# Kernel optimization log

Hardware: AMD Instinct MI355X
Metric: run time of the kernel (lower is better)

## Reference

```python
import jax, jax.numpy as jnp
import numpy as np

N, E, G = 50000, 640000, 128
IN_DIM, LAT, H, HID, NC = 128, 32, 8, 128, 2


def setup_inputs() -> dict:
    key = jax.random.key(0)
    ks = jax.random.split(key, 16)
    x = jax.random.normal(ks[0], (N, IN_DIM), dtype=jnp.float32)
    edge_index = jax.random.randint(ks[1], (2, E), 0, N, dtype=jnp.int64)
    # contiguous graph blocks covering all G graph ids
    batch = (jnp.arange(N, dtype=jnp.int64) * G) // N
    y = jax.random.randint(ks[2], (G,), 0, NC, dtype=jnp.int64)

    def lin(k, fi, fo):
        return jax.random.normal(k, (fi, fo), dtype=jnp.float32) / np.sqrt(fi)

    return {
        'x': x, 'edge_index': edge_index, 'batch': batch, 'y': y,
        'W1': lin(ks[3], IN_DIM, LAT), 'b1': jnp.zeros((LAT,), jnp.float32),
        'Wg1': lin(ks[4], LAT, H * LAT),
        'asrc1': jax.random.normal(ks[5], (H, LAT), jnp.float32) / np.sqrt(LAT),
        'adst1': jax.random.normal(ks[6], (H, LAT), jnp.float32) / np.sqrt(LAT),
        'bg1': jnp.zeros((H * LAT,), jnp.float32),
        'Wg2': lin(ks[7], H * LAT, H * LAT),
        'asrc2': jax.random.normal(ks[8], (H, LAT), jnp.float32) / np.sqrt(LAT),
        'adst2': jax.random.normal(ks[9], (H, LAT), jnp.float32) / np.sqrt(LAT),
        'bg2': jnp.zeros((H * LAT,), jnp.float32),
        'Wl1': lin(ks[10], LAT + 2 * H * LAT, HID), 'bl1': jnp.zeros((HID,), jnp.float32),
        'Wl2': lin(ks[11], HID, NC), 'bl2': jnp.zeros((NC,), jnp.float32),
    }


def _add_self_loops(edge_index, n):
    loop = jnp.arange(n, dtype=edge_index.dtype)
    row = jnp.concatenate([edge_index[0], loop])
    col = jnp.concatenate([edge_index[1], loop])
    return row, col


def gcn_conv(x, row, col, W, b):
    h = x @ W  # [N, C]
    deg = jax.ops.segment_sum(jnp.ones_like(col, dtype=h.dtype), col, num_segments=N)
    dinv = jax.lax.rsqrt(jnp.maximum(deg, 1.0))  # self-loops guarantee deg >= 1
    norm = dinv[row] * dinv[col]  # [E']
    return jax.ops.segment_sum(norm[:, None] * h[row], col, num_segments=N) + b


def gat_conv(x, row, col, W, a_src, a_dst, b):
    h = (x @ W).reshape(N, H, LAT)  # [N, H, C]
    s = jnp.einsum('nhc,hc->nh', h, a_src)
    d = jnp.einsum('nhc,hc->nh', h, a_dst)
    logits = jax.nn.leaky_relu(s[row] + d[col], negative_slope=0.2)  # [E', H]
    m = jax.ops.segment_max(logits, col, num_segments=N)
    m = jnp.where(jnp.isfinite(m), m, 0.0)
    e = jnp.exp(logits - m[col])
    z = jax.ops.segment_sum(e, col, num_segments=N)
    alpha = e / (z[col] + 1e-16)  # segment softmax over incoming edges
    out = jax.ops.segment_sum(alpha[:, :, None] * h[row], col, num_segments=N)
    return out.reshape(N, H * LAT) + b


def reference(x, edge_index, batch, y, W1, b1, Wg1, asrc1, adst1, bg1,
              Wg2, asrc2, adst2, bg2, Wl1, bl1, Wl2, bl2):
    row, col = _add_self_loops(edge_index, N)
    h1 = jax.nn.elu(gcn_conv(x, row, col, W1, b1))
    h2 = jax.nn.elu(gat_conv(h1, row, col, Wg1, asrc1, adst1, bg1))
    h3 = jax.nn.elu(gat_conv(h2, row, col, Wg2, asrc2, adst2, bg2))
    cat = jnp.concatenate([h1, h2, h3], axis=1)  # [N, 544]
    # first node of each graph (batch is sorted, contiguous blocks)
    idx = jnp.searchsorted(batch, jnp.arange(G, dtype=batch.dtype))
    feature = cat[idx] @ Wl1 + bl1  # [G, HID]
    hidden = jax.nn.elu(feature)  # eval mode: dropout off
    raw = hidden @ Wl2 + bl2
    prob = jax.nn.softmax(raw, axis=1)
    logits = jax.nn.log_softmax(raw, axis=1)
    loss = -jnp.mean(jnp.take_along_axis(logits, y[:, None], axis=1))
    pred = jnp.argmax(logits, axis=1, keepdims=True)
    return logits, loss, pred, prob, feature
```

## Files before the change

### kernel.cpp

```cpp
#include <hip/hip_runtime.h>
#include <math.h>

#define NN 50000
#define EE 640000
#define EP (EE + NN)
#define GG 128
#define IND 128
#define LATC 32
#define HH 8
#define HLC 256
#define HIDN 128
#define SCAN_B 256
#define SCAN_G ((NN + SCAN_B - 1) / SCAN_B)

typedef unsigned short ushortT;
typedef unsigned int uintT;
typedef short bf16x8 __attribute__((ext_vector_type(8)));
typedef float f32x4 __attribute__((ext_vector_type(4)));

__device__ __forceinline__ float elu1(float v) { return v > 0.f ? v : (__expf(v) - 1.f); }

__device__ __forceinline__ ushortT f2bf(float f) {
  unsigned int u = __float_as_uint(f);
  return (ushortT)((u + 0x7fffu + ((u >> 16) & 1u)) >> 16);
}
__device__ __forceinline__ float bf2f(ushortT s) {
  return __uint_as_float(((unsigned int)s) << 16);
}

__global__ void init_kernel(int* cnt, int* cursor) {
  int t = blockIdx.x * blockDim.x + threadIdx.x;
  if (t < NN) { cnt[t] = 1; cursor[t] = 0; }
}

__global__ void count_kernel(const int* col, int* cnt) {
  int t = blockIdx.x * blockDim.x + threadIdx.x;
  if (t < EE) atomicAdd(&cnt[col[t]], 1);
}

__global__ void scan_part_kernel(const int* __restrict__ cnt,
                                 int* __restrict__ bsum) {
  int t = threadIdx.x;
  int i = blockIdx.x * SCAN_B + t;
  int v = (i < NN) ? cnt[i] : 0;
#pragma unroll
  for (int d = 1; d < 64; d <<= 1) v += __shfl_xor(v, d);
  __shared__ int ws[4];
  if ((t & 63) == 0) ws[t >> 6] = v;
  __syncthreads();
  if (t == 0) bsum[blockIdx.x] = ws[0] + ws[1] + ws[2] + ws[3];
}

__global__ void scan_top_kernel(const int* __restrict__ bsum,
                                int* __restrict__ ebsum,
                                int* __restrict__ offs_last) {
  int t = threadIdx.x;
  int v = (t < SCAN_G) ? bsum[t] : 0;
  int orig = v;
  int lane = t & 63, w = t >> 6;
#pragma unroll
  for (int d = 1; d < 64; d <<= 1) {
    int o = __shfl_up(v, d);
    if (lane >= d) v += o;
  }
  __shared__ int ws[4];
  if (lane == 63) ws[w] = v;
  __syncthreads();
  int add = 0;
  for (int j = 0; j < w; ++j) add += ws[j];
  v += add;
  if (t < SCAN_G) ebsum[t] = v - orig;
  if (t == SCAN_G - 1) *offs_last = v;
}

__global__ void scan_final_kernel(const int* __restrict__ cnt,
                                  const int* __restrict__ ebsum,
                                  int* __restrict__ offs,
                                  float* __restrict__ dinv) {
  int t = threadIdx.x;
  int i = blockIdx.x * SCAN_B + t;
  int v = (i < NN) ? cnt[i] : 0;
  int orig = v;
  int lane = t & 63, w = t >> 6;
#pragma unroll
  for (int d = 1; d < 64; d <<= 1) {
    int o = __shfl_up(v, d);
    if (lane >= d) v += o;
  }
  __shared__ int ws[4];
  if (lane == 63) ws[w] = v;
  __syncthreads();
  int add = ebsum[blockIdx.x];
  for (int j = 0; j < w; ++j) add += ws[j];
  if (i < NN) {
    offs[i] = v - orig + add;
    dinv[i] = 1.f / sqrtf((float)orig);
  }
}

__global__ void build_kernel(const int* row, const int* col, const int* offs,
                             int* cursor, int* srcs) {
  int t = blockIdx.x * blockDim.x + threadIdx.x;
  if (t >= EP) return;
  int r, c;
  if (t < EE) { r = row[t]; c = col[t]; } else { r = t - EE; c = r; }
  int pos = offs[c] + atomicAdd(&cursor[c], 1);
  srcs[pos] = r;
}

__global__ void finalize_kernel(const int* offs, int* srcs) {
  int gw = (blockIdx.x * blockDim.x + threadIdx.x) >> 6;
  if (gw >= NN) return;
  int lane = threadIdx.x & 63;
  int beg = offs[gw], end = offs[gw + 1];
  int deg = end - beg;
  if (deg <= 64) {
    int v = (lane < deg) ? srcs[beg + lane] : 0x7fffffff;
    for (int k = 2; k <= 64; k <<= 1)
      for (int j = k >> 1; j > 0; j >>= 1) {
        int o = __shfl_xor(v, j);
        bool keepmin = (((lane & k) == 0) == ((lane & j) == 0));
        v = keepmin ? (v < o ? v : o) : (v > o ? v : o);
      }
    if (lane < deg) srcs[beg + lane] = v;
  } else if (lane == 0) {
    for (int i = beg + 1; i < end; ++i) {
      int v = srcs[i]; int j = i - 1;
      while (j >= beg && srcs[j] > v) { srcs[j + 1] = srcs[j]; --j; }
      srcs[j + 1] = v;
    }
  }
}

__launch_bounds__(256)
__global__ void gemm_in_kernel(const float* __restrict__ A,
                               const float* __restrict__ W,
                               float* __restrict__ out) {
  __shared__ float As[IND][68];
  __shared__ float Bs[IND][LATC];
  int bm = blockIdx.x * 64;
  int tid = threadIdx.x;
  int tx = tid & 31, ty = tid >> 5;
  {
    const float4* Wv = (const float4*)W;
    float4* Bv = (float4*)Bs;
#pragma unroll
    for (int i = 0; i < 4; ++i) Bv[tid + i * 256] = Wv[tid + i * 256];
  }
  {
    int m = tid >> 2, k4 = (tid & 3) * 4;
    int gm = bm + m;
#pragma unroll
    for (int pass = 0; pass < 8; ++pass) {
      int k = pass * 16 + k4;
      float4 v = make_float4(0.f, 0.f, 0.f, 0.f);
      if (gm < NN) v = *(const float4*)(A + (size_t)gm * IND + k);
      As[k + 0][m] = v.x; As[k + 1][m] = v.y;
      As[k + 2][m] = v.z; As[k + 3][m] = v.w;
    }
  }
  __syncthreads();
  float acc[8] = {};
#pragma unroll 8
  for (int kk = 0; kk < IND; ++kk) {
    float4 a0 = *(const float4*)(&As[kk][ty * 8]);
    float4 a1 = *(const float4*)(&As[kk][ty * 8 + 4]);
    float b = Bs[kk][tx];
    acc[0] += a0.x * b; acc[1] += a0.y * b; acc[2] += a0.z * b; acc[3] += a0.w * b;
    acc[4] += a1.x * b; acc[5] += a1.y * b; acc[6] += a1.z * b; acc[7] += a1.w * b;
  }
#pragma unroll
  for (int i = 0; i < 8; ++i) {
    int gm = bm + ty * 8 + i;
    if (gm < NN) out[(size_t)gm * LATC + tx] = acc[i];
  }
}

__global__ void wsplit_kernel(const float* __restrict__ Wg2,
                              ushortT* __restrict__ WhT,
                              ushortT* __restrict__ WlT) {
  int idx = blockIdx.x * 256 + threadIdx.x;
  if (idx >= HLC * HLC) return;
  int k = idx >> 8, n = idx & 255;
  float f = Wg2[idx];
  ushortT hi = f2bf(f);
  WhT[n * HLC + k] = hi;
  WlT[n * HLC + k] = f2bf(f - bf2f(hi));
}

__launch_bounds__(256)
__global__ void gemm_gat2_mfma(const float* __restrict__ A,
                               const ushortT* __restrict__ WhT,
                               const ushortT* __restrict__ WlT,
                               const float* __restrict__ asrc,
                               const float* __restrict__ adst,
                               ushortT* __restrict__ hgb,
                               float* __restrict__ sbuf,
                               float* __restrict__ dbuf) {
  __shared__ __align__(16) char smem[51200];
  ushortT* Ah = (ushortT*)smem;
  ushortT* Al = Ah + 64 * 40;
  ushortT* Bh = (ushortT*)(smem + 10240);
  ushortT* Bl = Bh + 256 * 40;
  float* LDSf = (float*)(smem + 10240);

  int tid = threadIdx.x;
  int lane = tid & 63;
  int w = tid >> 6;
  int l15 = lane & 15, lg = lane >> 4;
  int bm = blockIdx.x * 64;

  f32x4 zero4 = {0.f, 0.f, 0.f, 0.f};
  f32x4 acc[4][4];
#pragma unroll
  for (int mi = 0; mi < 4; ++mi)
#pragma unroll
    for (int ni = 0; ni < 4; ++ni) acc[mi][ni] = zero4;

  for (int k0 = 0; k0 < HLC; k0 += 32) {
    {
      int row = tid >> 2, kb = (tid & 3) * 8;
      int gm = bm + row;
      float f[8];
      if (gm < NN) {
        float4 u0 = *(const float4*)(A + (size_t)gm * HLC + k0 + kb);
        float4 u1 = *(const float4*)(A + (size_t)gm * HLC + k0 + kb + 4);
        f[0] = u0.x; f[1] = u0.y; f[2] = u0.z; f[3] = u0.w;
        f[4] = u1.x; f[5] = u1.y; f[6] = u1.z; f[7] = u1.w;
      } else {
#pragma unroll
        for (int j = 0; j < 8; ++j) f[j] = 0.f;
      }
      bf16x8 vh, vl;
#pragma unroll
      for (int j = 0; j < 8; ++j) {
        ushortT hi = f2bf(f[j]);
        vh[j] = (short)hi;
        vl[j] = (short)f2bf(f[j] - bf2f(hi));
      }
      *(bf16x8*)(Ah + row * 40 + kb) = vh;
      *(bf16x8*)(Al + row * 40 + kb) = vl;
    }
    {
      const bf16x8* ph = (const bf16x8*)(WhT + (size_t)tid * HLC + k0);
      const bf16x8* pl = (const bf16x8*)(WlT + (size_t)tid * HLC + k0);
#pragma unroll
      for (int i = 0; i < 4; ++i) {
        *(bf16x8*)(Bh + tid * 40 + i * 8) = ph[i];
        *(bf16x8*)(Bl + tid * 40 + i * 8) = pl[i];
      }
    }
    __syncthreads();
    bf16x8 ah[4], al[4], bh[4], bl[4];
#pragma unroll
    for (int mi = 0; mi < 4; ++mi) {
      int off = (mi * 16 + l15) * 40 + lg * 8;
      ah[mi] = *(const bf16x8*)(Ah + off);
      al[mi] = *(const bf16x8*)(Al + off);
    }
#pragma unroll
    for (int ni = 0; ni < 4; ++ni) {
      int off = (w * 64 + ni * 16 + l15) * 40 + lg * 8;
      bh[ni] = *(const bf16x8*)(Bh + off);
      bl[ni] = *(const bf16x8*)(Bl + off);
    }
#pragma unroll
    for (int mi = 0; mi < 4; ++mi)
#pragma unroll
      for (int ni = 0; ni < 4; ++ni) {
        acc[mi][ni] = __builtin_amdgcn_mfma_f32_16x16x32_bf16(
            al[mi], bh[ni], acc[mi][ni], 0, 0, 0);
        acc[mi][ni] = __builtin_amdgcn_mfma_f32_16x16x32_bf16(
            ah[mi], bl[ni], acc[mi][ni], 0, 0, 0);
        acc[mi][ni] = __builtin_amdgcn_mfma_f32_16x16x32_bf16(
            ah[mi], bh[ni], acc[mi][ni], 0, 0, 0);
      }
    __syncthreads();
  }

  float av[4], bv[4];
#pragma unroll
  for (int ni = 0; ni < 4; ++ni) {
    int c = w * 64 + ni * 16 + l15;
    av[ni] = asrc[c];
    bv[ni] = adst[c];
  }
#pragma unroll
  for (int mi = 0; mi < 4; ++mi)
#pragma unroll
    for (int r = 0; r < 4; ++r) {
      int gm = bm + mi * 16 + lg * 4 + r;
      float s0 = acc[mi][0][r] * av[0] + acc[mi][1][r] * av[1];
      float s1 = acc[mi][2][r] * av[2] + acc[mi][3][r] * av[3];
      float d0 = acc[mi][0][r] * bv[0] + acc[mi][1][r] * bv[1];
      float d1 = acc[mi][2][r] * bv[2] + acc[mi][3][r] * bv[3];
#pragma unroll
      for (int m = 1; m <= 8; m <<= 1) {
        s0 += __shfl_xor(s0, m);
        s1 += __shfl_xor(s1, m);
        d0 += __shfl_xor(d0, m);
        d1 += __shfl_xor(d1, m);
      }
      if (l15 == 0 && gm < NN) {
        sbuf[gm * HH + 2 * w] = s0;
        sbuf[gm * HH + 2 * w + 1] = s1;
        dbuf[gm * HH + 2 * w] = d0;
        dbuf[gm * HH + 2 * w + 1] = d1;
      }
    }

#pragma unroll
  for (int p = 0; p < 2; ++p) {
    __syncthreads();
#pragma unroll
    for (int q = 0; q < 2; ++q) {
      int mi = 2 * p + q;
#pragma unroll
      for (int ni = 0; ni < 4; ++ni)
#pragma unroll
        for (int r = 0; r < 4; ++r) {
          int lrow = q * 16 + lg * 4 + r;
          LDSf[lrow * 260 + w * 64 + ni * 16 + l15] = acc[mi][ni][r];
        }
    }
    __syncthreads();
    int row = tid >> 3, cb = (tid & 7) * 32;
    int gm = bm + p * 32 + row;
    if (gm < NN) {
      uintT u[16];
#pragma unroll
      for (int i = 0; i < 8; ++i) {
        float4 v = *(const float4*)(LDSf + row * 260 + cb + i * 4);
        u[2 * i] = (uintT)f2bf(v.x) | ((uintT)f2bf(v.y) << 16);
        u[2 * i + 1] = (uintT)f2bf(v.z) | ((uintT)f2bf(v.w) << 16);
      }
      uintT* dst = (uintT*)(hgb + (size_t)gm * HLC + cb);
#pragma unroll
      for (int i = 0; i < 4; ++i) {
        uint4 s;
        s.x = u[4 * i]; s.y = u[4 * i + 1];
        s.z = u[4 * i + 2]; s.w = u[4 * i + 3];
        *(uint4*)(dst + 4 * i) = s;
      }
    }
  }
}

__global__ void gcn_agg_kernel(const float* __restrict__ hW, const int* offs,
                               const int* srcs, const float* dinv,
                               const float* b1, float* h1) {
  int wid = (blockIdx.x * blockDim.x + threadIdx.x) >> 6;
  if (wid >= NN) return;
  int lane = threadIdx.x & 63;
  int c = lane & 31, half = lane >> 5;
  int beg = offs[wid], end = offs[wid + 1];
  float acc = 0.f;
  for (int p = beg + half; p < end; p += 2) {
    int src = srcs[p];
    acc += dinv[src] * hW[src * LATC + c];
  }
  acc += __shfl_xor(acc, 32);
  if (lane < 32) {
    float v = dinv[wid] * acc + b1[c];
    h1[wid * LATC + c] = elu1(v);
  }
}

__global__ void sd1_kernel(const float* __restrict__ h1,
                           const float* __restrict__ Wg1,
                           const float* __restrict__ asrc,
                           const float* __restrict__ adst, float* s,
                           float* d) {
  __shared__ float va[HLC], vb[HLC];
  int t = threadIdx.x;
  {
    int c = t & 31, h = t >> 5;
    float sa = 0.f, sb = 0.f;
#pragma unroll 8
    for (int j = 0; j < 32; ++j) {
      float w = Wg1[(size_t)c * HLC + h * 32 + j];
      sa += w * asrc[h * 32 + j];
      sb += w * adst[h * 32 + j];
    }
    va[t] = sa;
    vb[t] = sb;
  }
  __syncthreads();
  int idx = blockIdx.x * 256 + t;
  if (idx >= NN * HH) return;
  int n = idx >> 3, h = idx & 7;
  const float4* hv = (const float4*)(h1 + (size_t)n * LATC);
  const float4* av = (const float4*)(va + h * LATC);
  const float4* bv = (const float4*)(vb + h * LATC);
  float ss = 0.f, dd = 0.f;
#pragma unroll
  for (int i = 0; i < 8; ++i) {
    float4 xx = hv[i], aa = av[i], bb = bv[i];
    ss += xx.x * aa.x + xx.y * aa.y + xx.z * aa.z + xx.w * aa.w;
    dd += xx.x * bb.x + xx.y * bb.y + xx.z * bb.z + xx.w * bb.w;
  }
  s[idx] = ss; d[idx] = dd;
}

__global__ void gat1_agg_kernel(const float* __restrict__ h1,
                                const float* __restrict__ s,
                                const float* __restrict__ dd, const int* offs,
                                const int* srcs, float* __restrict__ agg) {
  int wid = (blockIdx.x * blockDim.x + threadIdx.x) >> 6;
  if (wid >= NN) return;
  int lane = threadIdx.x & 63;
  int h = lane >> 3, c4 = (lane & 7) * 4;
  int beg = offs[wid], end = offs[wid + 1];
  float dn = dd[wid * HH + h];
  float self = s[wid * HH + h] + dn;
  float m = self > 0.f ? self : 0.2f * self;
  float z = 0.f;
  float ax = 0.f, ay = 0.f, az = 0.f, aw = 0.f;
#pragma unroll 4
  for (int p = beg; p < end; ++p) {
    int src = srcs[p];
    float sv = s[src * HH + h] + dn;
    float logit = sv > 0.f ? sv : 0.2f * sv;
    float e = __expf(logit - m);
    z += e;
    float4 v = *(const float4*)(h1 + (size_t)src * LATC + c4);
    ax += e * v.x; ay += e * v.y; az += e * v.z; aw += e * v.w;
  }
  float zinv = 1.f / (z + 1e-16f);
  *(float4*)(agg + (size_t)wid * HLC + h * LATC + c4) =
      make_float4(ax * zinv, ay * zinv, az * zinv, aw * zinv);
}

__launch_bounds__(256)
__global__ void gat1_proj_kernel(const float* __restrict__ agg,
                                 const float* __restrict__ Wg1,
                                 const float* __restrict__ bg,
                                 float* __restrict__ h2) {
  __shared__ float As[HLC][32];
  __shared__ float Ws[32][HLC];
  int bm = blockIdx.x * 32;
  int t = threadIdx.x;
  {
    const float4* Wv = (const float4*)Wg1;
    float4* Bv = (float4*)Ws;
#pragma unroll
    for (int i = 0; i < 8; ++i) Bv[t + i * 256] = Wv[t + i * 256];
  }
  {
    int n = t & 31, cb = (t >> 5) * 32;
    int gm = bm + n;
#pragma unroll
    for (int j = 0; j < 8; ++j) {
      float4 v = make_float4(0.f, 0.f, 0.f, 0.f);
      if (gm < NN) v = *(const float4*)(agg + (size_t)gm * HLC + cb + j * 4);
      As[cb + j * 4 + 0][n] = v.x;
      As[cb + j * 4 + 1][n] = v.y;
      As[cb + j * 4 + 2][n] = v.z;
      As[cb + j * 4 + 3][n] = v.w;
    }
  }
  __syncthreads();
  int tx = t & 31, ty = t >> 5;
  int h1o = (tx >> 3) * 32;
  int h2o = 128 + (tx >> 3) * 32;
  float acc1[4][4] = {}, acc2[4][4] = {};
#pragma unroll 4
  for (int kk = 0; kk < 32; ++kk) {
    float4 a1 = *(const float4*)(&As[h1o + kk][ty * 4]);
    float4 a2 = *(const float4*)(&As[h2o + kk][ty * 4]);
    float4 w1 = *(const float4*)(&Ws[kk][tx * 4]);
    float4 w2 = *(const float4*)(&Ws[kk][128 + tx * 4]);
    float ar1[4] = {a1.x, a1.y, a1.z, a1.w};
    float ar2[4] = {a2.x, a2.y, a2.z, a2.w};
    float wr1[4] = {w1.x, w1.y, w1.z, w1.w};
    float wr2[4] = {w2.x, w2.y, w2.z, w2.w};
#pragma unroll
    for (int r = 0; r < 4; ++r)
#pragma unroll
      for (int q = 0; q < 4; ++q) {
        acc1[r][q] += ar1[r] * wr1[q];
        acc2[r][q] += ar2[r] * wr2[q];
      }
  }
  float4 b1 = *(const float4*)(bg + tx * 4);
  float4 b2 = *(const float4*)(bg + 128 + tx * 4);
  float bb1[4] = {b1.x, b1.y, b1.z, b1.w};
  float bb2[4] = {b2.x, b2.y, b2.z, b2.w};
#pragma unroll
  for (int r = 0; r < 4; ++r) {
    int gm = bm + ty * 4 + r;
    if (gm >= NN) continue;
    float4 o1, o2;
    o1.x = elu1(acc1[r][0] + bb1[0]); o1.y = elu1(acc1[r][1] + bb1[1]);
    o1.z = elu1(acc1[r][2] + bb1[2]); o1.w = elu1(acc1[r][3] + bb1[3]);
    o2.x = elu1(acc2[r][0] + bb2[0]); o2.y = elu1(acc2[r][1] + bb2[1]);
    o2.z = elu1(acc2[r][2] + bb2[2]); o2.w = elu1(acc2[r][3] + bb2[3]);
    *(float4*)(h2 + (size_t)gm * HLC + tx * 4) = o1;
    *(float4*)(h2 + (size_t)gm * HLC + 128 + tx * 4) = o2;
  }
}

__global__ void gat_agg_kernel(const ushortT* __restrict__ hgb,
                               const float* __restrict__ s,
                               const float* __restrict__ dd, const int* offs,
                               const int* srcs, const float* bg, float* out) {
  int wid = (blockIdx.x * blockDim.x + threadIdx.x) >> 6;
  if (wid >= NN) return;
  int lane = threadIdx.x & 63;
  int hh = lane >> 3;
  int ch = lane << 2;
  int beg = offs[wid], end = offs[wid + 1];
  float dn = dd[wid * HH + hh];
  float self = s[wid * HH + hh] + dn;
  float m = self > 0.f ? self : 0.2f * self;
  float z = 0.f;
  float ax = 0.f, ay = 0.f, az = 0.f, aw = 0.f;
#pragma unroll 4
  for (int p = beg; p < end; ++p) {
    int src = srcs[p];
    float xv = s[src * HH + hh] + dn;
    float logit = xv > 0.f ? xv : 0.2f * xv;
    float e = __expf(logit - m);
    z += e;
    ushort4 v = *(const ushort4*)(hgb + (size_t)src * HLC + ch);
    ax += e * bf2f(v.x); ay += e * bf2f(v.y);
    az += e * bf2f(v.z); aw += e * bf2f(v.w);
  }
  float zinv = 1.f / (z + 1e-16f);
  float4 bb = *(const float4*)(bg + ch);
  float4 o;
  o.x = elu1(ax * zinv + bb.x); o.y = elu1(ay * zinv + bb.y);
  o.z = elu1(az * zinv + bb.z); o.w = elu1(aw * zinv + bb.w);
  *(float4*)(out + (size_t)wid * HLC + ch) = o;
}

__global__ void head_kernel(const float* __restrict__ h1,
                            const float* __restrict__ h2,
                            const float* __restrict__ h3, const int* batch,
                            const int* y, const float* __restrict__ Wl1,
                            const float* bl1, const float* __restrict__ Wl2,
                            const float* bl2, float* out, float* lterms) {
  int g = blockIdx.x, tid = threadIdx.x;
  __shared__ float cat[544];
  __shared__ float hidden[HIDN];
  __shared__ float raw_s[2];
  __shared__ int idx_s;
  if (tid == 0) {
    int lo = 0, hi = NN;
    while (lo < hi) { int mid = (lo + hi) >> 1; if (batch[mid] < g) lo = mid + 1; else hi = mid; }
    idx_s = lo;
  }
  __syncthreads();
  int idx = idx_s;
  if (tid < 32) cat[tid] = h1[idx * LATC + tid];
  for (int i = tid; i < HLC; i += HIDN) {
    cat[32 + i] = h2[(size_t)idx * HLC + i];
    cat[288 + i] = h3[(size_t)idx * HLC + i];
  }
  __syncthreads();
  float f = bl1[tid];
  for (int k = 0; k < 544; ++k) f += cat[k] * Wl1[k * HIDN + tid];
  out[641 + g * HIDN + tid] = f;
  hidden[tid] = elu1(f);
  __syncthreads();
  if (tid < 2) {
    float r = bl2[tid];
    for (int j = 0; j < HIDN; ++j) r += hidden[j] * Wl2[j * 2 + tid];
    raw_s[tid] = r;
  }
  __syncthreads();
  if (tid == 0) {
    float r0 = raw_s[0], r1 = raw_s[1];
    float mx = fmaxf(r0, r1);
    float e0 = expf(r0 - mx), e1 = expf(r1 - mx);
    float zz = e0 + e1;
    float lse = mx + logf(zz);
    float lg0 = r0 - lse, lg1 = r1 - lse;
    out[g * 2 + 0] = lg0; out[g * 2 + 1] = lg1;
    out[385 + g * 2 + 0] = e0 / zz; out[385 + g * 2 + 1] = e1 / zz;
    out[257 + g] = (r1 > r0) ? 1.f : 0.f;
    lterms[g] = -((y[g] == 0) ? lg0 : lg1);
  }
}

__global__ void loss_kernel(const float* lterms, float* out) {
  __shared__ float buf[GG];
  int tid = threadIdx.x;
  buf[tid] = lterms[tid];
  __syncthreads();
  for (int off = GG / 2; off > 0; off >>= 1) {
    if (tid < off) buf[tid] += buf[tid + off];
    __syncthreads();
  }
  if (tid == 0) out[256] = buf[0] / (float)GG;
}

extern "C" void kernel_launch(void* const* d_in, const int* in_sizes, int n_in,
                              void* d_out, int out_size, void* d_ws,
                              size_t ws_size, hipStream_t stream) {
  const float* x = (const float*)d_in[0];
  const int* ei = (const int*)d_in[1];
  const int* batch = (const int*)d_in[2];
  const int* y = (const int*)d_in[3];
  const float* W1 = (const float*)d_in[4];
  const float* b1 = (const float*)d_in[5];
  const float* Wg1 = (const float*)d_in[6];
  const float* asrc1 = (const float*)d_in[7];
  const float* adst1 = (const float*)d_in[8];
  const float* bg1 = (const float*)d_in[9];
  const float* Wg2 = (const float*)d_in[10];
  const float* asrc2 = (const float*)d_in[11];
  const float* adst2 = (const float*)d_in[12];
  const float* bg2 = (const float*)d_in[13];
  const float* Wl1 = (const float*)d_in[14];
  const float* bl1 = (const float*)d_in[15];
  const float* Wl2 = (const float*)d_in[16];
  const float* bl2 = (const float*)d_in[17];
  float* out = (float*)d_out;

  const int* erow = ei;
  const int* ecol = ei + EE;

  char* p = (char*)d_ws;
  auto alloc = [&](size_t bytes) {
    void* r = (void*)p;
    p += (bytes + 255) & ~(size_t)255;
    return r;
  };
  int* cnt = (int*)alloc(NN * 4);
  int* offs = (int*)alloc((NN + 1) * 4);
  int* cursor = (int*)alloc(NN * 4);
  int* srcs = (int*)alloc((size_t)EP * 4);
  int* bsum = (int*)alloc(SCAN_G * 4);
  int* ebsum = (int*)alloc(SCAN_G * 4);
  float* dinv = (float*)alloc(NN * 4);
  float* hW = (float*)alloc((size_t)NN * LATC * 4);
  float* h1 = (float*)alloc((size_t)NN * LATC * 4);
  float* hg = (float*)alloc((size_t)NN * HLC * 4);
  float* h2 = (float*)alloc((size_t)NN * HLC * 4);
  float* h3 = (float*)alloc((size_t)NN * HLC * 4);
  float* sbuf = (float*)alloc((size_t)NN * HH * 4);
  float* dbuf = (float*)alloc((size_t)NN * HH * 4);
  float* lterms = (float*)alloc(GG * 4);
  ushortT* whT = (ushortT*)alloc((size_t)HLC * HLC * 2);
  ushortT* wlT = (ushortT*)alloc((size_t)HLC * HLC * 2);
  ushortT* hgb = (ushortT*)hg;

  const int NBLK = (NN + 63) / 64;

  init_kernel<<<(NN + 255) / 256, 256, 0, stream>>>(cnt, cursor);
  count_kernel<<<(EE + 255) / 256, 256, 0, stream>>>(ecol, cnt);
  scan_part_kernel<<<SCAN_G, SCAN_B, 0, stream>>>(cnt, bsum);
  scan_top_kernel<<<1, 256, 0, stream>>>(bsum, ebsum, offs + NN);
  scan_final_kernel<<<SCAN_G, SCAN_B, 0, stream>>>(cnt, ebsum, offs, dinv);
  build_kernel<<<(EP + 255) / 256, 256, 0, stream>>>(erow, ecol, offs, cursor, srcs);
  finalize_kernel<<<(NN + 3) / 4, 256, 0, stream>>>(offs, srcs);

  wsplit_kernel<<<(HLC * HLC + 255) / 256, 256, 0, stream>>>(Wg2, whT, wlT);

  gemm_in_kernel<<<NBLK, 256, 0, stream>>>(x, W1, hW);
  gcn_agg_kernel<<<(NN + 3) / 4, 256, 0, stream>>>(hW, offs, srcs, dinv, b1, h1);

  sd1_kernel<<<(NN * HH + 255) / 256, 256, 0, stream>>>(h1, Wg1, asrc1, adst1,
                                                        sbuf, dbuf);
  gat1_agg_kernel<<<(NN + 3) / 4, 256, 0, stream>>>(h1, sbuf, dbuf, offs, srcs, hg);
  gat1_proj_kernel<<<(NN + 31) / 32, 256, 0, stream>>>(hg, Wg1, bg1, h2);

  gemm_gat2_mfma<<<NBLK, 256, 0, stream>>>(h2, whT, wlT, asrc2, adst2, hgb,
                                           sbuf, dbuf);
  gat_agg_kernel<<<(NN + 3) / 4, 256, 0, stream>>>(hgb, sbuf, dbuf, offs, srcs, bg2, h3);

  head_kernel<<<GG, HIDN, 0, stream>>>(h1, h2, h3, batch, y, Wl1, bl1, Wl2, bl2,
                                       out, lterms);
  loss_kernel<<<1, GG, 0, stream>>>(lterms, out);
}
```

Before: 378.0 us.

## Retile input GEMM, split GAT1 aggregation edges across half-waves, memset init

```diff
diff --git a/kernel.cpp b/kernel.cpp
--- a/kernel.cpp
+++ b/kernel.cpp
@@ -28,11 +28,6 @@
   return __uint_as_float(((unsigned int)s) << 16);
 }
 
-__global__ void init_kernel(int* cnt, int* cursor) {
-  int t = blockIdx.x * blockDim.x + threadIdx.x;
-  if (t < NN) { cnt[t] = 1; cursor[t] = 0; }
-}
-
 __global__ void count_kernel(const int* col, int* cnt) {
   int t = blockIdx.x * blockDim.x + threadIdx.x;
   if (t < EE) atomicAdd(&cnt[col[t]], 1);
@@ -42,7 +37,7 @@
                                  int* __restrict__ bsum) {
   int t = threadIdx.x;
   int i = blockIdx.x * SCAN_B + t;
-  int v = (i < NN) ? cnt[i] : 0;
+  int v = (i < NN) ? cnt[i] + 1 : 0;
 #pragma unroll
   for (int d = 1; d < 64; d <<= 1) v += __shfl_xor(v, d);
   __shared__ int ws[4];
@@ -79,7 +74,7 @@
                                   float* __restrict__ dinv) {
   int t = threadIdx.x;
   int i = blockIdx.x * SCAN_B + t;
-  int v = (i < NN) ? cnt[i] : 0;
+  int v = (i < NN) ? cnt[i] + 1 : 0;
   int orig = v;
   int lane = t & 63, w = t >> 6;
 #pragma unroll
@@ -136,43 +131,51 @@
 __global__ void gemm_in_kernel(const float* __restrict__ A,
                                const float* __restrict__ W,
                                float* __restrict__ out) {
-  __shared__ float As[IND][68];
-  __shared__ float Bs[IND][LATC];
-  int bm = blockIdx.x * 64;
+  __shared__ float As[32][264];
+  __shared__ float Bs[32][32];
+  int bm = blockIdx.x * 256;
   int tid = threadIdx.x;
-  int tx = tid & 31, ty = tid >> 5;
-  {
-    const float4* Wv = (const float4*)W;
-    float4* Bv = (float4*)Bs;
-#pragma unroll
-    for (int i = 0; i < 4; ++i) Bv[tid + i * 256] = Wv[tid + i * 256];
-  }
-  {
-    int m = tid >> 2, k4 = (tid & 3) * 4;
-    int gm = bm + m;
-#pragma unroll
-    for (int pass = 0; pass < 8; ++pass) {
-      int k = pass * 16 + k4;
-      float4 v = make_float4(0.f, 0.f, 0.f, 0.f);
-      if (gm < NN) v = *(const float4*)(A + (size_t)gm * IND + k);
-      As[k + 0][m] = v.x; As[k + 1][m] = v.y;
-      As[k + 2][m] = v.z; As[k + 3][m] = v.w;
-    }
-  }
-  __syncthreads();
-  float acc[8] = {};
-#pragma unroll 8
-  for (int kk = 0; kk < IND; ++kk) {
-    float4 a0 = *(const float4*)(&As[kk][ty * 8]);
-    float4 a1 = *(const float4*)(&As[kk][ty * 8 + 4]);
-    float b = Bs[kk][tx];
-    acc[0] += a0.x * b; acc[1] += a0.y * b; acc[2] += a0.z * b; acc[3] += a0.w * b;
-    acc[4] += a1.x * b; acc[5] += a1.y * b; acc[6] += a1.z * b; acc[7] += a1.w * b;
+  int tx = tid & 7, ty = tid >> 3;
+  float acc[8][4] = {};
+  for (int k0 = 0; k0 < IND; k0 += 32) {
+    {
+      int gm = bm + tid;
+      bool ok = gm < NN;
+#pragma unroll
+      for (int j = 0; j < 8; ++j) {
+        float4 v = ok ? *(const float4*)(A + (size_t)gm * IND + k0 + j * 4)
+                      : make_float4(0.f, 0.f, 0.f, 0.f);
+        As[j * 4 + 0][tid] = v.x; As[j * 4 + 1][tid] = v.y;
+        As[j * 4 + 2][tid] = v.z; As[j * 4 + 3][tid] = v.w;
+      }
+    }
+#pragma unroll
+    for (int j = 0; j < 4; ++j) {
+      int idx = tid + j * 256;
+      int kk = idx >> 5, c = idx & 31;
+      Bs[kk][c] = W[(size_t)(k0 + kk) * LATC + c];
+    }
+    __syncthreads();
+#pragma unroll 4
+    for (int kk = 0; kk < 32; ++kk) {
+      float4 a0 = *(const float4*)(&As[kk][ty * 8]);
+      float4 a1 = *(const float4*)(&As[kk][ty * 8 + 4]);
+      float4 b = *(const float4*)(&Bs[kk][tx * 4]);
+      float ar[8] = {a0.x, a0.y, a0.z, a0.w, a1.x, a1.y, a1.z, a1.w};
+      float bc[4] = {b.x, b.y, b.z, b.w};
+#pragma unroll
+      for (int i = 0; i < 8; ++i)
+#pragma unroll
+        for (int j = 0; j < 4; ++j) acc[i][j] += ar[i] * bc[j];
+    }
+    __syncthreads();
   }
 #pragma unroll
   for (int i = 0; i < 8; ++i) {
     int gm = bm + ty * 8 + i;
-    if (gm < NN) out[(size_t)gm * LATC + tx] = acc[i];
+    if (gm < NN)
+      *(float4*)(out + (size_t)gm * LATC + tx * 4) =
+          make_float4(acc[i][0], acc[i][1], acc[i][2], acc[i][3]);
   }
 }
 
@@ -409,26 +412,38 @@
   int wid = (blockIdx.x * blockDim.x + threadIdx.x) >> 6;
   if (wid >= NN) return;
   int lane = threadIdx.x & 63;
-  int h = lane >> 3, c4 = (lane & 7) * 4;
+  int g = lane >> 5;
+  int l5 = lane & 31;
+  int h = l5 >> 2;
+  int c8 = (l5 & 3) * 8;
   int beg = offs[wid], end = offs[wid + 1];
   float dn = dd[wid * HH + h];
   float self = s[wid * HH + h] + dn;
   float m = self > 0.f ? self : 0.2f * self;
   float z = 0.f;
-  float ax = 0.f, ay = 0.f, az = 0.f, aw = 0.f;
-#pragma unroll 4
-  for (int p = beg; p < end; ++p) {
+  float a[8] = {};
+#pragma unroll 2
+  for (int p = beg + g; p < end; p += 2) {
     int src = srcs[p];
     float sv = s[src * HH + h] + dn;
     float logit = sv > 0.f ? sv : 0.2f * sv;
     float e = __expf(logit - m);
     z += e;
-    float4 v = *(const float4*)(h1 + (size_t)src * LATC + c4);
-    ax += e * v.x; ay += e * v.y; az += e * v.z; aw += e * v.w;
-  }
-  float zinv = 1.f / (z + 1e-16f);
-  *(float4*)(agg + (size_t)wid * HLC + h * LATC + c4) =
-      make_float4(ax * zinv, ay * zinv, az * zinv, aw * zinv);
+    float4 v0 = *(const float4*)(h1 + (size_t)src * LATC + c8);
+    float4 v1 = *(const float4*)(h1 + (size_t)src * LATC + c8 + 4);
+    a[0] += e * v0.x; a[1] += e * v0.y; a[2] += e * v0.z; a[3] += e * v0.w;
+    a[4] += e * v1.x; a[5] += e * v1.y; a[6] += e * v1.z; a[7] += e * v1.w;
+  }
+  z += __shfl_xor(z, 32);
+#pragma unroll
+  for (int j = 0; j < 8; ++j) a[j] += __shfl_xor(a[j], 32);
+  if (g == 0) {
+    float zinv = 1.f / (z + 1e-16f);
+    *(float4*)(agg + (size_t)wid * HLC + h * LATC + c8) =
+        make_float4(a[0] * zinv, a[1] * zinv, a[2] * zinv, a[3] * zinv);
+    *(float4*)(agg + (size_t)wid * HLC + h * LATC + c8 + 4) =
+        make_float4(a[4] * zinv, a[5] * zinv, a[6] * zinv, a[7] * zinv);
+  }
 }
 
 __launch_bounds__(256)
@@ -627,9 +642,10 @@
     p += (bytes + 255) & ~(size_t)255;
     return r;
   };
-  int* cnt = (int*)alloc(NN * 4);
+  int* cntcur = (int*)alloc((size_t)2 * NN * 4);
+  int* cnt = cntcur;
+  int* cursor = cntcur + NN;
   int* offs = (int*)alloc((NN + 1) * 4);
-  int* cursor = (int*)alloc(NN * 4);
   int* srcs = (int*)alloc((size_t)EP * 4);
   int* bsum = (int*)alloc(SCAN_G * 4);
   int* ebsum = (int*)alloc(SCAN_G * 4);
@@ -648,7 +664,7 @@
 
   const int NBLK = (NN + 63) / 64;
 
-  init_kernel<<<(NN + 255) / 256, 256, 0, stream>>>(cnt, cursor);
+  hipMemsetAsync(cntcur, 0, (size_t)2 * NN * 4, stream);
   count_kernel<<<(EE + 255) / 256, 256, 0, stream>>>(ecol, cnt);
   scan_part_kernel<<<SCAN_G, SCAN_B, 0, stream>>>(cnt, bsum);
   scan_top_kernel<<<1, 256, 0, stream>>>(bsum, ebsum, offs + NN);
@@ -658,7 +674,7 @@
 
   wsplit_kernel<<<(HLC * HLC + 255) / 256, 256, 0, stream>>>(Wg2, whT, wlT);
 
-  gemm_in_kernel<<<NBLK, 256, 0, stream>>>(x, W1, hW);
+  gemm_in_kernel<<<(NN + 255) / 256, 256, 0, stream>>>(x, W1, hW);
   gcn_agg_kernel<<<(NN + 3) / 4, 256, 0, stream>>>(hW, offs, srcs, dinv, b1, h1);
 
   sd1_kernel<<<(NN * HH + 255) / 256, 256, 0, stream>>>(h1, Wg1, asrc1, adst1,
```

Measured after the change: 375.3 us. No clear change (-0.7%).
